# Optimization experiments

Hardware: AMD Instinct MI355X
Metric: run time of the kernel (lower is better)

Reference implementation:

```python
import jax, jax.numpy as jnp
import numpy as np

H, D, K = 8, 512, 64
EPS = 1e-12


def _l2norm(x):
    # F.normalize(p=2, dim=-1): x / max(||x||_2, eps)
    n = jnp.sqrt(jnp.sum(x * x, axis=-1, keepdims=True))
    return x / jnp.maximum(n, EPS)


def setup_inputs() -> dict:
    key = jax.random.key(0)
    ks = jax.random.split(key, 8)
    S, B = 1024, 16
    scale = 1.0 / np.sqrt(D)
    return {
        "query": jax.random.normal(ks[0], (S, B, D), dtype=jnp.float32),
        "key": jax.random.normal(ks[1], (S, B, D), dtype=jnp.float32),
        "value": jax.random.normal(ks[2], (S, B, D), dtype=jnp.float32),
        # stacked per-head projection weights, torch Linear convention [out,in]
        "WQ": jax.random.uniform(ks[3], (H, K, D), jnp.float32, -scale, scale),
        "WK": jax.random.uniform(ks[4], (H, K, D), jnp.float32, -scale, scale),
        "WV": jax.random.uniform(ks[5], (H, K, D), jnp.float32, -scale, scale),
        "Wout": jax.random.uniform(ks[6], (D, H * K), jnp.float32,
                                   -1.0 / np.sqrt(H * K), 1.0 / np.sqrt(H * K)),
    }


def reference(query, key, value, WQ, WK, WV, Wout):
    temp = K ** 0.5
    # project all heads at once: [S,B,D] x [H,K,D] -> [B,H,S,K]
    wq = _l2norm(jnp.einsum("sbd,hkd->bhsk", query, WQ))
    wk = _l2norm(jnp.einsum("sbd,hkd->bhsk", key, WK))
    wv = _l2norm(jnp.einsum("sbd,hkd->bhsk", value, WV))
    # cosine-similarity attention scores [B,H,Sq,Sk]
    scores = jnp.einsum("bhsk,bhtk->bhst", wq, wk) / temp
    aff = jax.nn.softmax(scores, axis=-1)
    out = jnp.einsum("bhst,bhtk->bhsk", aff, wv)  # [B,H,S,K]
    # concat heads -> [S,B,H*K] (matches torch per-head concat on last dim)
    Sq, B = query.shape[0], query.shape[1]
    concat = out.transpose(2, 0, 1, 3).reshape(Sq, B, H * K)
    return concat @ Wout.T  # [S,B,D]
```

## Files before the change

kernel.cpp:

```cpp
#include <hip/hip_runtime.h>
#include <cstdint>
#include <cstddef>

typedef unsigned int u32;
typedef unsigned short u16;
typedef __attribute__((ext_vector_type(8))) short short8;
typedef __attribute__((ext_vector_type(4))) float f32x4;

#define S_LEN 1024
#define BATCH 16
#define NHEAD 8
#define DMODEL 512
#define KHD 64
#define NROW (S_LEN * BATCH)

__device__ __forceinline__ u16 f2bf(float f) {
    u32 u = __float_as_uint(f);
    return (u16)((u + 0x7fffu + ((u >> 16) & 1u)) >> 16);
}

__device__ __forceinline__ void gl_lds16(const void* g, void* l) {
    __builtin_amdgcn_global_load_lds(
        (const __attribute__((address_space(1))) void*)(uintptr_t)g,
        (__attribute__((address_space(3))) void*)(uintptr_t)l, 16, 0, 0);
}

__global__ __launch_bounds__(256) void wcvt_kernel(
    const float* __restrict__ WQ, const float* __restrict__ WK,
    const float* __restrict__ WV, const float* __restrict__ Wo,
    u16* __restrict__ dst)
{
    const int m = blockIdx.y;
    const float* __restrict__ src = (m == 0) ? WQ : (m == 1) ? WK : (m == 2) ? WV : Wo;
    const int idx = (blockIdx.x * 256 + threadIdx.x) * 4;
    const float4 v = *(const float4*)(src + idx);
    u16 r[4];
    r[0] = f2bf(v.x); r[1] = f2bf(v.y); r[2] = f2bf(v.z); r[3] = f2bf(v.w);
    *(uint2*)(dst + (size_t)m * DMODEL * DMODEL + idx) = *(uint2*)r;
}

__global__ __launch_bounds__(512, 4) void proj_kernel(
    const float* __restrict__ q, const float* __restrict__ k,
    const float* __restrict__ v, const u16* __restrict__ Wb,
    u16* __restrict__ outN)
{
    __shared__ __align__(16) u16 Alds[2][128 * 64];
    __shared__ __align__(16) u16 Blds[2][128 * 64];

    const int tid  = threadIdx.x;
    const int wave = tid >> 6;
    const int lane = tid & 63;
    const int m16  = lane & 15;
    const int quad = lane >> 4;
    const int wm   = wave >> 1;
    const int wn   = wave & 1;

    const int bid  = blockIdx.x;
    const bool isM1 = bid < 1024;
    int z, bx, by, bb;
    if (isM1) { z = bid >> 9; by = (bid >> 7) & 3; bx = bid & 127; bb = 0; }
    else { const int r = bid - 1024; z = 2; bb = r >> 5; by = (r >> 3) & 3; bx = r & 7; }

    const int row0 = bx * 128;
    const int n0   = by * 128;
    const float* __restrict__ A32 = isM1 ? (z ? k : q) : (v + (size_t)bb * DMODEL);
    const size_t astr = isM1 ? (size_t)DMODEL : (size_t)BATCH * DMODEL;
    const u16* __restrict__ B = Wb + (size_t)z * DMODEL * DMODEL;

    f32x4 acc[2][4] = {};

    const int arow = wave * 16 + (lane >> 2);
    const int ac0  = lane & 3;
    const float* __restrict__ aPtr = A32 + (size_t)(row0 + arow) * astr;
    const int brow   = lane >> 3;
    const int bchunk = (lane & 7) ^ brow;

    float4 pA[4], pB[4];

#define LOADA(kt, rg)                                                           \
    {                                                                           \
        _Pragma("unroll")                                                       \
        for (int j = 0; j < 4; j++)                                             \
            rg[j] = *(const float4*)(aPtr + (kt) + (ac0 + 4 * j) * 4);          \
    }
#define WRITEA(rg, bufi)                                                        \
    {                                                                           \
        _Pragma("unroll")                                                       \
        for (int j = 0; j < 4; j++) {                                           \
            const int c = ac0 + 4 * j;                                          \
            u32 lo, hi;                                                         \
            asm("v_cvt_pk_bf16_f32 %0, %1, %2" : "=v"(lo) : "v"(rg[j].x), "v"(rg[j].y)); \
            asm("v_cvt_pk_bf16_f32 %0, %1, %2" : "=v"(hi) : "v"(rg[j].z), "v"(rg[j].w)); \
            uint2 pk; pk.x = lo; pk.y = hi;                                     \
            *(uint2*)&Alds[bufi][arow * 64 + (((c >> 1) ^ (arow & 7)) << 3) +   \
                                 ((c & 1) << 2)] = pk;                          \
        }                                                                       \
    }
#define STAGEB(kt, bufi)                                                        \
    {                                                                           \
        const u16* bp = B + (size_t)(n0 + wave * 16 + brow) * DMODEL + (kt) +   \
                        bchunk * 8;                                             \
        u16* lb = &Blds[bufi][(wave * 16) * 64];                                \
        gl_lds16(bp, lb);                                                       \
        gl_lds16(bp + (size_t)8 * DMODEL, lb + 8 * 64);                         \
    }

    auto compute = [&](int bufi) {
#pragma unroll
        for (int half = 0; half < 2; half++) {
            short8 af[2], bfr[4];
#pragma unroll
            for (int mt = 0; mt < 2; mt++)
                af[mt] = *(const short8*)&Alds[bufi][(wm * 32 + mt * 16 + m16) * 64 +
                                                     (((half << 2) + quad) ^ (m16 & 7)) * 8];
#pragma unroll
            for (int nt = 0; nt < 4; nt++)
                bfr[nt] = *(const short8*)&Blds[bufi][(wn * 64 + nt * 16 + m16) * 64 +
                                                      (((half << 2) + quad) ^ (m16 & 7)) * 8];
#pragma unroll
            for (int mt = 0; mt < 2; mt++)
#pragma unroll
                for (int nt = 0; nt < 4; nt++)
                    acc[mt][nt] = __builtin_amdgcn_mfma_f32_16x16x32_bf16(af[mt], bfr[nt], acc[mt][nt], 0, 0, 0);
        }
    };

    LOADA(0, pA)
    STAGEB(0, 0)
    LOADA(64, pB)
    STAGEB(64, 1)
    asm volatile("s_waitcnt vmcnt(6)" ::: "memory");
    __builtin_amdgcn_sched_barrier(0);
    WRITEA(pA, 0)
    asm volatile("s_waitcnt lgkmcnt(0)" ::: "memory");
    __builtin_amdgcn_s_barrier();
    __builtin_amdgcn_sched_barrier(0);

#pragma unroll
    for (int t = 0; t < 8; t++) {
        compute(t & 1);
        if (t < 6) {
            __builtin_amdgcn_s_barrier();
            __builtin_amdgcn_sched_barrier(0);
            if (t & 1) { LOADA((t + 2) * 64, pB) }
            else       { LOADA((t + 2) * 64, pA) }
            STAGEB((t + 2) * 64, t & 1);
        }
        if (t < 7) {
            if (t < 6) asm volatile("s_waitcnt vmcnt(6)" ::: "memory");
            else       asm volatile("s_waitcnt vmcnt(0)" ::: "memory");
            __builtin_amdgcn_sched_barrier(0);
            if ((t + 1) & 1) { WRITEA(pB, 1) }
            else             { WRITEA(pA, 0) }
            asm volatile("s_waitcnt lgkmcnt(0)" ::: "memory");
            __builtin_amdgcn_s_barrier();
            __builtin_amdgcn_sched_barrier(0);
        }
    }
#undef LOADA
#undef WRITEA
#undef STAGEB

    const int h = (n0 >> 6) + wn;
    u16* outZ = outN + (size_t)z * ((size_t)BATCH * NHEAD * S_LEN * KHD);
    if (isM1) {
#pragma unroll
        for (int mt = 0; mt < 2; mt++) {
#pragma unroll
            for (int r = 0; r < 4; r++) {
                float ss = 0.0f;
#pragma unroll
                for (int nt = 0; nt < 4; nt++) ss += acc[mt][nt][r] * acc[mt][nt][r];
                ss += __shfl_xor(ss, 1);
                ss += __shfl_xor(ss, 2);
                ss += __shfl_xor(ss, 4);
                ss += __shfl_xor(ss, 8);
                const float sc = 1.0f / fmaxf(sqrtf(ss), 1e-12f);
                const int i = row0 + wm * 32 + mt * 16 + quad * 4 + r;
                const int s = i >> 4, bq = i & 15;
                u16* op = outZ + (((size_t)bq * NHEAD + h) * S_LEN + s) * KHD;
#pragma unroll
                for (int nt = 0; nt < 4; nt++)
                    op[nt * 16 + m16] = f2bf(acc[mt][nt][r] * sc);
            }
        }
    } else {
#pragma unroll
        for (int mt = 0; mt < 2; mt++) {
            float scl[4];
#pragma unroll
            for (int r = 0; r < 4; r++) {
                float ss = 0.0f;
#pragma unroll
                for (int nt = 0; nt < 4; nt++) ss += acc[mt][nt][r] * acc[mt][nt][r];
                ss += __shfl_xor(ss, 1);
                ss += __shfl_xor(ss, 2);
                ss += __shfl_xor(ss, 4);
                ss += __shfl_xor(ss, 8);
                scl[r] = 1.0f / fmaxf(sqrtf(ss), 1e-12f);
            }
            const int sbase = row0 + wm * 32 + mt * 16 + quad * 4;
#pragma unroll
            for (int nt = 0; nt < 4; nt++) {
                const int vcol = nt * 16 + m16;
                uint2 pk;
                pk.x = (u32)f2bf(acc[mt][nt][0] * scl[0]) |
                       ((u32)f2bf(acc[mt][nt][1] * scl[1]) << 16);
                pk.y = (u32)f2bf(acc[mt][nt][2] * scl[2]) |
                       ((u32)f2bf(acc[mt][nt][3] * scl[3]) << 16);
                u16* dp = outZ + (((size_t)bb * NHEAD + h) * KHD + vcol) * S_LEN + sbase;
                *(uint2*)dp = pk;
            }
        }
    }
}

__global__ __launch_bounds__(512, 2) void gemm_out_kernel(
    const u16* __restrict__ Abf,
    const u16* __restrict__ Wb,
    float* __restrict__ outP)
{
    __shared__ __align__(16) u16 Alds[2][128 * 64];
    __shared__ __align__(16) u16 Blds[2][128 * 64];

    const int tid  = threadIdx.x;
    const int wave = tid >> 6;
    const int lane = tid & 63;
    const int m16  = lane & 15;
    const int quad = lane >> 4;
    const int wm   = wave >> 1;
    const int wn   = wave & 1;
    const int n0   = blockIdx.y * 128;
    const int row0 = blockIdx.x * 128;

    const int brow   = lane >> 3;
    const int bchunk = (lane & 7) ^ brow;

    f32x4 acc[2][4] = {};

    auto stage = [&](int kt, int b) {
        const int colc = kt + bchunk * 8;
        const int hh   = colc >> 6;
        const int kk   = colc & 63;
        u16* la = &Alds[b][(wave * 16) * 64];
#pragma unroll
        for (int j = 0; j < 2; j++) {
            const int i  = row0 + wave * 16 + j * 8 + brow;
            const int ss = i >> 4, bx = i & 15;
            gl_lds16(Abf + (((size_t)(bx * NHEAD + hh) * S_LEN + ss) * KHD + kk),
                     la + j * 8 * 64);
        }
        const u16* bp = Wb + (size_t)(n0 + wave * 16 + brow) * DMODEL + kt + bchunk * 8;
        u16* lb = &Blds[b][(wave * 16) * 64];
#pragma unroll
        for (int j = 0; j < 2; j++)
            gl_lds16(bp + (size_t)j * 8 * DMODEL, lb + j * 8 * 64);
    };
    auto compute = [&](int b) {
#pragma unroll
        for (int half = 0; half < 2; half++) {
            short8 af[2], bfr[4];
#pragma unroll
            for (int mt = 0; mt < 2; mt++)
                af[mt] = *(const short8*)&Alds[b][(wm * 32 + mt * 16 + m16) * 64 +
                                                  (((half << 2) + quad) ^ (m16 & 7)) * 8];
#pragma unroll
            for (int nt = 0; nt < 4; nt++)
                bfr[nt] = *(const short8*)&Blds[b][(wn * 64 + nt * 16 + m16) * 64 +
                                                   (((half << 2) + quad) ^ (m16 & 7)) * 8];
#pragma unroll
            for (int mt = 0; mt < 2; mt++)
#pragma unroll
                for (int nt = 0; nt < 4; nt++)
                    acc[mt][nt] = __builtin_amdgcn_mfma_f32_16x16x32_bf16(af[mt], bfr[nt], acc[mt][nt], 0, 0, 0);
        }
    };

    stage(0, 0);
    stage(64, 1);
    asm volatile("s_waitcnt vmcnt(4)" ::: "memory");
    __builtin_amdgcn_s_barrier();
    __builtin_amdgcn_sched_barrier(0);

#pragma unroll
    for (int t = 0; t < 8; t++) {
        compute(t & 1);
        if (t < 6) {
            __builtin_amdgcn_s_barrier();
            __builtin_amdgcn_sched_barrier(0);
            stage((t + 2) * 64, t & 1);
        }
        if (t < 7) {
            if (t < 6) asm volatile("s_waitcnt vmcnt(4)" ::: "memory");
            else       asm volatile("s_waitcnt vmcnt(0)" ::: "memory");
            __builtin_amdgcn_s_barrier();
            __builtin_amdgcn_sched_barrier(0);
        }
    }

#pragma unroll
    for (int mt = 0; mt < 2; mt++) {
#pragma unroll
        for (int r = 0; r < 4; r++) {
            const int i = row0 + wm * 32 + mt * 16 + quad * 4 + r;
            float* op = outP + (size_t)i * DMODEL + n0 + wn * 64;
#pragma unroll
            for (int nt = 0; nt < 4; nt++)
                op[nt * 16 + m16] = acc[mt][nt][r];
        }
    }
}

__global__ __launch_bounds__(256, 2) void attn_kernel(
    const u16* __restrict__ wq, const u16* __restrict__ wk, const u16* __restrict__ wvT,
    u16* __restrict__ Xout)
{
    __shared__ __align__(16) u16 Klds[2][64 * 64];
    __shared__ __align__(16) u16 Vlds[2][64 * 64];
    __shared__ __align__(16) u16 Plds[4][4][16 * 32];

    const int tid  = threadIdx.x;
    const int wave = tid >> 6;
    const int lane = tid & 63;
    const int m16  = lane & 15;
    const int quad = lane >> 4;
    const int bh   = blockIdx.x;
    const int qt   = blockIdx.y;

    const u16* Qb = wq  + (size_t)bh * S_LEN * KHD;
    const u16* Kb = wk  + (size_t)bh * S_LEN * KHD;
    const u16* Vb = wvT + (size_t)bh * KHD * S_LEN;

    const int qr0 = qt * 256 + wave * 64;
    short8 qf[4][2];
#pragma unroll
    for (int qb = 0; qb < 4; qb++) {
        qf[qb][0] = *(const short8*)(Qb + (size_t)(qr0 + qb * 16 + m16) * KHD + quad * 8);
        qf[qb][1] = *(const short8*)(Qb + (size_t)(qr0 + qb * 16 + m16) * KHD + 32 + quad * 8);
    }

    short8 ones;
#pragma unroll
    for (int j = 0; j < 8; j++) ones[j] = (short)0x3F80;

    f32x4 o[4][4] = {};
    f32x4 ls[4]   = {};
    const float C1 = 0.125f, C2 = 0.0078125f;

    const int srow   = lane >> 3;
    const int schunk = (lane & 7) ^ srow;
    const int r0     = wave * 8 + srow;
    const int pswz   = (m16 >> 1) & 3;

    gl_lds16(Kb + (size_t)r0 * KHD + schunk * 8,               &Klds[0][(wave * 8) * 64]);
    gl_lds16(Kb + (size_t)(r0 + 32) * KHD + schunk * 8,        &Klds[0][(wave * 8 + 32) * 64]);
    gl_lds16(Vb + (size_t)r0 * S_LEN + schunk * 8,             &Vlds[0][(wave * 8) * 64]);
    gl_lds16(Vb + (size_t)(r0 + 32) * S_LEN + schunk * 8,      &Vlds[0][(wave * 8 + 32) * 64]);
    __syncthreads();

    for (int it = 0; it < S_LEN / 64; it++) {
        const int cur = it & 1;

        if (it + 1 < S_LEN / 64) {
            const int nxt = cur ^ 1;
            const int kt0 = (it + 1) * 64;
            gl_lds16(Kb + (size_t)(kt0 + r0) * KHD + schunk * 8,        &Klds[nxt][(wave * 8) * 64]);
            gl_lds16(Kb + (size_t)(kt0 + r0 + 32) * KHD + schunk * 8,   &Klds[nxt][(wave * 8 + 32) * 64]);
            gl_lds16(Vb + (size_t)r0 * S_LEN + kt0 + schunk * 8,        &Vlds[nxt][(wave * 8) * 64]);
            gl_lds16(Vb + (size_t)(r0 + 32) * S_LEN + kt0 + schunk * 8, &Vlds[nxt][(wave * 8 + 32) * 64]);
        }

#pragma unroll
        for (int cc = 0; cc < 2; cc++) {
#pragma unroll
            for (int mm = 0; mm < 2; mm++) {
                const int mt = cc * 2 + mm;
                const short8 kf0 = *(const short8*)&Klds[cur][(mt * 16 + m16) * 64 + (quad ^ (m16 & 7)) * 8];
                const short8 kf1 = *(const short8*)&Klds[cur][(mt * 16 + m16) * 64 + ((4 + quad) ^ (m16 & 7)) * 8];
#pragma unroll
                for (int qb = 0; qb < 4; qb++) {
                    f32x4 s = {};
                    s = __builtin_amdgcn_mfma_f32_16x16x32_bf16(kf0, qf[qb][0], s, 0, 0, 0);
                    s = __builtin_amdgcn_mfma_f32_16x16x32_bf16(kf1, qf[qb][1], s, 0, 0, 0);
                    u32 up[4];
#pragma unroll
                    for (int r = 0; r < 4; r++) {
                        const float y = s[r];
                        const float p = fmaf(fmaf(C2, y, C1), y, 1.0f);
                        up[r] = __float_as_uint(p);
                    }
                    uint2 pk;
                    pk.x = __builtin_amdgcn_perm(up[1], up[0], 0x07060302u);
                    pk.y = __builtin_amdgcn_perm(up[3], up[2], 0x07060302u);
                    *(uint2*)((char*)&Plds[wave][qb][0] + m16 * 64 +
                              ((((mm << 1) + (quad >> 1)) ^ pswz) << 4) + ((quad & 1) << 3)) = pk;
                }
            }

            short8 vfr[4];
#pragma unroll
            for (int vt = 0; vt < 4; vt++)
                vfr[vt] = *(const short8*)&Vlds[cur][(vt * 16 + m16) * 64 +
                                                     (((cc << 2) + quad) ^ (m16 & 7)) * 8];
            __builtin_amdgcn_s_setprio(1);
#pragma unroll
            for (int qb = 0; qb < 4; qb++) {
                const short8 pb = *(const short8*)((const char*)&Plds[wave][qb][0] + m16 * 64 +
                                                   ((quad ^ pswz) << 4));
                ls[qb] = __builtin_amdgcn_mfma_f32_16x16x32_bf16(ones, pb, ls[qb], 0, 0, 0);
#pragma unroll
                for (int vt = 0; vt < 4; vt++)
                    o[qb][vt] = __builtin_amdgcn_mfma_f32_16x16x32_bf16(vfr[vt], pb, o[qb][vt], 0, 0, 0);
            }
            __builtin_amdgcn_s_setprio(0);
        }

        __syncthreads();
    }

    u16* outB = Xout + (size_t)bh * S_LEN * KHD;
#pragma unroll
    for (int qb = 0; qb < 4; qb++) {
        const float inv = 1.0f / ls[qb][0];
        const int qrow = qr0 + qb * 16 + m16;
        u16* cp = outB + (size_t)qrow * KHD;
#pragma unroll
        for (int vt = 0; vt < 4; vt++) {
            uint2 pk;
            pk.x = (u32)f2bf(o[qb][vt][0] * inv) | ((u32)f2bf(o[qb][vt][1] * inv) << 16);
            pk.y = (u32)f2bf(o[qb][vt][2] * inv) | ((u32)f2bf(o[qb][vt][3] * inv) << 16);
            *(uint2*)(cp + vt * 16 + quad * 4) = pk;
        }
    }
}

extern "C" void kernel_launch(void* const* d_in, const int* in_sizes, int n_in,
                              void* d_out, int out_size, void* d_ws, size_t ws_size,
                              hipStream_t stream) {
    const float* q    = (const float*)d_in[0];
    const float* k    = (const float*)d_in[1];
    const float* v    = (const float*)d_in[2];
    const float* WQ   = (const float*)d_in[3];
    const float* WK   = (const float*)d_in[4];
    const float* WV   = (const float*)d_in[5];
    const float* Wout = (const float*)d_in[6];
    float* out = (float*)d_out;

    const size_t per = (size_t)BATCH * NHEAD * S_LEN * KHD;
    u16* wsQKV = (u16*)d_ws;
    u16* wsW   = wsQKV + 3 * per;

    wcvt_kernel<<<dim3(256, 4), 256, 0, stream>>>(WQ, WK, WV, Wout, wsW);

    proj_kernel<<<dim3(1536), 512, 0, stream>>>(q, k, v, wsW, wsQKV);

    attn_kernel<<<dim3(BATCH * NHEAD, S_LEN / 256), 256, 0, stream>>>(
        wsQKV, wsQKV + per, wsQKV + 2 * per, wsQKV);

    gemm_out_kernel<<<dim3(NROW / 128, DMODEL / 128), 512, 0, stream>>>(
        wsQKV, wsW + (size_t)3 * DMODEL * DMODEL, out);
}
```

Before: 241.4 us.

## Fuse weight bf16 conversion into GEMM loaders and drop separate conversion kernel

```diff
diff --git a/kernel.cpp b/kernel.cpp
--- a/kernel.cpp
+++ b/kernel.cpp
@@ -25,23 +25,11 @@
         (__attribute__((address_space(3))) void*)(uintptr_t)l, 16, 0, 0);
 }
 
-__global__ __launch_bounds__(256) void wcvt_kernel(
-    const float* __restrict__ WQ, const float* __restrict__ WK,
-    const float* __restrict__ WV, const float* __restrict__ Wo,
-    u16* __restrict__ dst)
-{
-    const int m = blockIdx.y;
-    const float* __restrict__ src = (m == 0) ? WQ : (m == 1) ? WK : (m == 2) ? WV : Wo;
-    const int idx = (blockIdx.x * 256 + threadIdx.x) * 4;
-    const float4 v = *(const float4*)(src + idx);
-    u16 r[4];
-    r[0] = f2bf(v.x); r[1] = f2bf(v.y); r[2] = f2bf(v.z); r[3] = f2bf(v.w);
-    *(uint2*)(dst + (size_t)m * DMODEL * DMODEL + idx) = *(uint2*)r;
-}
-
 __global__ __launch_bounds__(512, 4) void proj_kernel(
     const float* __restrict__ q, const float* __restrict__ k,
-    const float* __restrict__ v, const u16* __restrict__ Wb,
+    const float* __restrict__ v,
+    const float* __restrict__ WQ, const float* __restrict__ WK,
+    const float* __restrict__ WV,
     u16* __restrict__ outN)
 {
     __shared__ __align__(16) u16 Alds[2][128 * 64];
@@ -65,50 +53,48 @@
     const int n0   = by * 128;
     const float* __restrict__ A32 = isM1 ? (z ? k : q) : (v + (size_t)bb * DMODEL);
     const size_t astr = isM1 ? (size_t)DMODEL : (size_t)BATCH * DMODEL;
-    const u16* __restrict__ B = Wb + (size_t)z * DMODEL * DMODEL;
+    const float* __restrict__ B32 = (z == 0) ? WQ : (z == 1) ? WK : WV;
 
     f32x4 acc[2][4] = {};
 
-    const int arow = wave * 16 + (lane >> 2);
-    const int ac0  = lane & 3;
-    const float* __restrict__ aPtr = A32 + (size_t)(row0 + arow) * astr;
-    const int brow   = lane >> 3;
-    const int bchunk = (lane & 7) ^ brow;
+    const int srow = wave * 16 + (lane >> 2);
+    const int sc0  = lane & 3;
+    const float* __restrict__ aPtr = A32 + (size_t)(row0 + srow) * astr;
+    const float* __restrict__ bPtr = B32 + (size_t)(n0 + srow) * DMODEL;
 
     float4 pA[4], pB[4];
+    float4 wA[4], wB[4];
 
 #define LOADA(kt, rg)                                                           \
     {                                                                           \
         _Pragma("unroll")                                                       \
         for (int j = 0; j < 4; j++)                                             \
-            rg[j] = *(const float4*)(aPtr + (kt) + (ac0 + 4 * j) * 4);          \
-    }
-#define WRITEA(rg, bufi)                                                        \
+            rg[j] = *(const float4*)(aPtr + (kt) + (sc0 + 4 * j) * 4);          \
+    }
+#define LOADB(kt, rg)                                                           \
+    {                                                                           \
+        _Pragma("unroll")                                                       \
+        for (int j = 0; j < 4; j++)                                             \
+            rg[j] = *(const float4*)(bPtr + (kt) + (sc0 + 4 * j) * 4);          \
+    }
+#define CVTWR(rg, lds, bufi)                                                    \
     {                                                                           \
         _Pragma("unroll")                                                       \
         for (int j = 0; j < 4; j++) {                                           \
-            const int c = ac0 + 4 * j;                                          \
+            const int c = sc0 + 4 * j;                                          \
             u32 lo, hi;                                                         \
             asm("v_cvt_pk_bf16_f32 %0, %1, %2" : "=v"(lo) : "v"(rg[j].x), "v"(rg[j].y)); \
             asm("v_cvt_pk_bf16_f32 %0, %1, %2" : "=v"(hi) : "v"(rg[j].z), "v"(rg[j].w)); \
             uint2 pk; pk.x = lo; pk.y = hi;                                     \
-            *(uint2*)&Alds[bufi][arow * 64 + (((c >> 1) ^ (arow & 7)) << 3) +   \
-                                 ((c & 1) << 2)] = pk;                          \
+            *(uint2*)&lds[bufi][srow * 64 + (((c >> 1) ^ (srow & 7)) << 3) +    \
+                               ((c & 1) << 2)] = pk;                            \
         }                                                                       \
     }
-#define STAGEB(kt, bufi)                                                        \
-    {                                                                           \
-        const u16* bp = B + (size_t)(n0 + wave * 16 + brow) * DMODEL + (kt) +   \
-                        bchunk * 8;                                             \
-        u16* lb = &Blds[bufi][(wave * 16) * 64];                                \
-        gl_lds16(bp, lb);                                                       \
-        gl_lds16(bp + (size_t)8 * DMODEL, lb + 8 * 64);                         \
-    }
 
     auto compute = [&](int bufi) {
+        short8 af[2], bfr[4];
 #pragma unroll
         for (int half = 0; half < 2; half++) {
-            short8 af[2], bfr[4];
 #pragma unroll
             for (int mt = 0; mt < 2; mt++)
                 af[mt] = *(const short8*)&Alds[bufi][(wm * 32 + mt * 16 + m16) * 64 +
@@ -117,21 +103,24 @@
             for (int nt = 0; nt < 4; nt++)
                 bfr[nt] = *(const short8*)&Blds[bufi][(wn * 64 + nt * 16 + m16) * 64 +
                                                       (((half << 2) + quad) ^ (m16 & 7)) * 8];
+            __builtin_amdgcn_s_setprio(1);
 #pragma unroll
             for (int mt = 0; mt < 2; mt++)
 #pragma unroll
                 for (int nt = 0; nt < 4; nt++)
                     acc[mt][nt] = __builtin_amdgcn_mfma_f32_16x16x32_bf16(af[mt], bfr[nt], acc[mt][nt], 0, 0, 0);
+            __builtin_amdgcn_s_setprio(0);
         }
     };
 
     LOADA(0, pA)
-    STAGEB(0, 0)
+    LOADB(0, wA)
     LOADA(64, pB)
-    STAGEB(64, 1)
-    asm volatile("s_waitcnt vmcnt(6)" ::: "memory");
+    LOADB(64, wB)
+    asm volatile("s_waitcnt vmcnt(8)" ::: "memory");
     __builtin_amdgcn_sched_barrier(0);
-    WRITEA(pA, 0)
+    CVTWR(pA, Alds, 0)
+    CVTWR(wA, Blds, 0)
     asm volatile("s_waitcnt lgkmcnt(0)" ::: "memory");
     __builtin_amdgcn_s_barrier();
     __builtin_amdgcn_sched_barrier(0);
@@ -142,24 +131,23 @@
         if (t < 6) {
             __builtin_amdgcn_s_barrier();
             __builtin_amdgcn_sched_barrier(0);
-            if (t & 1) { LOADA((t + 2) * 64, pB) }
-            else       { LOADA((t + 2) * 64, pA) }
-            STAGEB((t + 2) * 64, t & 1);
+            if (t & 1) { LOADA((t + 2) * 64, pB) LOADB((t + 2) * 64, wB) }
+            else       { LOADA((t + 2) * 64, pA) LOADB((t + 2) * 64, wA) }
         }
         if (t < 7) {
-            if (t < 6) asm volatile("s_waitcnt vmcnt(6)" ::: "memory");
+            if (t < 6) asm volatile("s_waitcnt vmcnt(8)" ::: "memory");
             else       asm volatile("s_waitcnt vmcnt(0)" ::: "memory");
             __builtin_amdgcn_sched_barrier(0);
-            if ((t + 1) & 1) { WRITEA(pB, 1) }
-            else             { WRITEA(pA, 0) }
+            if ((t + 1) & 1) { CVTWR(pB, Alds, 1) CVTWR(wB, Blds, 1) }
+            else             { CVTWR(pA, Alds, 0) CVTWR(wA, Blds, 0) }
             asm volatile("s_waitcnt lgkmcnt(0)" ::: "memory");
             __builtin_amdgcn_s_barrier();
             __builtin_amdgcn_sched_barrier(0);
         }
     }
 #undef LOADA
-#undef WRITEA
-#undef STAGEB
+#undef LOADB
+#undef CVTWR
 
     const int h = (n0 >> 6) + wn;
     u16* outZ = outN + (size_t)z * ((size_t)BATCH * NHEAD * S_LEN * KHD);
@@ -215,9 +203,9 @@
     }
 }
 
-__global__ __launch_bounds__(512, 2) void gemm_out_kernel(
+__global__ __launch_bounds__(512, 4) void gemm_out_kernel(
     const u16* __restrict__ Abf,
-    const u16* __restrict__ Wb,
+    const float* __restrict__ Wo32,
     float* __restrict__ outP)
 {
     __shared__ __align__(16) u16 Alds[2][128 * 64];
@@ -235,10 +223,14 @@
 
     const int brow   = lane >> 3;
     const int bchunk = (lane & 7) ^ brow;
+    const int srow = wave * 16 + (lane >> 2);
+    const int sc0  = lane & 3;
+    const float* __restrict__ bPtr = Wo32 + (size_t)(n0 + srow) * DMODEL;
 
     f32x4 acc[2][4] = {};
-
-    auto stage = [&](int kt, int b) {
+    float4 wA[4], wB[4];
+
+    auto stageA = [&](int kt, int b) {
         const int colc = kt + bchunk * 8;
         const int hh   = colc >> 6;
         const int kk   = colc & 63;
@@ -250,16 +242,30 @@
             gl_lds16(Abf + (((size_t)(bx * NHEAD + hh) * S_LEN + ss) * KHD + kk),
                      la + j * 8 * 64);
         }
-        const u16* bp = Wb + (size_t)(n0 + wave * 16 + brow) * DMODEL + kt + bchunk * 8;
-        u16* lb = &Blds[b][(wave * 16) * 64];
-#pragma unroll
-        for (int j = 0; j < 2; j++)
-            gl_lds16(bp + (size_t)j * 8 * DMODEL, lb + j * 8 * 64);
     };
+#define LOADB(kt, rg)                                                           \
+    {                                                                           \
+        _Pragma("unroll")                                                       \
+        for (int j = 0; j < 4; j++)                                             \
+            rg[j] = *(const float4*)(bPtr + (kt) + (sc0 + 4 * j) * 4);          \
+    }
+#define CVTWRB(rg, bufi)                                                        \
+    {                                                                           \
+        _Pragma("unroll")                                                       \
+        for (int j = 0; j < 4; j++) {                                           \
+            const int c = sc0 + 4 * j;                                          \
+            u32 lo, hi;                                                         \
+            asm("v_cvt_pk_bf16_f32 %0, %1, %2" : "=v"(lo) : "v"(rg[j].x), "v"(rg[j].y)); \
+            asm("v_cvt_pk_bf16_f32 %0, %1, %2" : "=v"(hi) : "v"(rg[j].z), "v"(rg[j].w)); \
+            uint2 pk; pk.x = lo; pk.y = hi;                                     \
+            *(uint2*)&Blds[bufi][srow * 64 + (((c >> 1) ^ (srow & 7)) << 3) +   \
+                                 ((c & 1) << 2)] = pk;                          \
+        }                                                                       \
+    }
     auto compute = [&](int b) {
+        short8 af[2], bfr[4];
 #pragma unroll
         for (int half = 0; half < 2; half++) {
-            short8 af[2], bfr[4];
 #pragma unroll
             for (int mt = 0; mt < 2; mt++)
                 af[mt] = *(const short8*)&Alds[b][(wm * 32 + mt * 16 + m16) * 64 +
@@ -268,17 +274,24 @@
             for (int nt = 0; nt < 4; nt++)
                 bfr[nt] = *(const short8*)&Blds[b][(wn * 64 + nt * 16 + m16) * 64 +
                                                    (((half << 2) + quad) ^ (m16 & 7)) * 8];
+            __builtin_amdgcn_s_setprio(1);
 #pragma unroll
             for (int mt = 0; mt < 2; mt++)
 #pragma unroll
                 for (int nt = 0; nt < 4; nt++)
                     acc[mt][nt] = __builtin_amdgcn_mfma_f32_16x16x32_bf16(af[mt], bfr[nt], acc[mt][nt], 0, 0, 0);
+            __builtin_amdgcn_s_setprio(0);
         }
     };
 
-    stage(0, 0);
-    stage(64, 1);
-    asm volatile("s_waitcnt vmcnt(4)" ::: "memory");
+    stageA(0, 0);
+    LOADB(0, wA)
+    stageA(64, 1);
+    LOADB(64, wB)
+    asm volatile("s_waitcnt vmcnt(6)" ::: "memory");
+    __builtin_amdgcn_sched_barrier(0);
+    CVTWRB(wA, 0)
+    asm volatile("s_waitcnt lgkmcnt(0)" ::: "memory");
     __builtin_amdgcn_s_barrier();
     __builtin_amdgcn_sched_barrier(0);
 
@@ -288,15 +301,23 @@
         if (t < 6) {
             __builtin_amdgcn_s_barrier();
             __builtin_amdgcn_sched_barrier(0);
-            stage((t + 2) * 64, t & 1);
+            stageA((t + 2) * 64, t & 1);
+            if (t & 1) { LOADB((t + 2) * 64, wB) }
+            else       { LOADB((t + 2) * 64, wA) }
         }
         if (t < 7) {
-            if (t < 6) asm volatile("s_waitcnt vmcnt(4)" ::: "memory");
+            if (t < 6) asm volatile("s_waitcnt vmcnt(6)" ::: "memory");
             else       asm volatile("s_waitcnt vmcnt(0)" ::: "memory");
+            __builtin_amdgcn_sched_barrier(0);
+            if ((t + 1) & 1) { CVTWRB(wB, 1) }
+            else             { CVTWRB(wA, 0) }
+            asm volatile("s_waitcnt lgkmcnt(0)" ::: "memory");
             __builtin_amdgcn_s_barrier();
             __builtin_amdgcn_sched_barrier(0);
         }
     }
+#undef LOADB
+#undef CVTWRB
 
 #pragma unroll
     for (int mt = 0; mt < 2; mt++) {
@@ -448,15 +469,12 @@
 
     const size_t per = (size_t)BATCH * NHEAD * S_LEN * KHD;
     u16* wsQKV = (u16*)d_ws;
-    u16* wsW   = wsQKV + 3 * per;
-
-    wcvt_kernel<<<dim3(256, 4), 256, 0, stream>>>(WQ, WK, WV, Wout, wsW);
-
-    proj_kernel<<<dim3(1536), 512, 0, stream>>>(q, k, v, wsW, wsQKV);
+
+    proj_kernel<<<dim3(1536), 512, 0, stream>>>(q, k, v, WQ, WK, WV, wsQKV);
 
     attn_kernel<<<dim3(BATCH * NHEAD, S_LEN / 256), 256, 0, stream>>>(
         wsQKV, wsQKV + per, wsQKV + 2 * per, wsQKV);
 
     gemm_out_kernel<<<dim3(NROW / 128, DMODEL / 128), 512, 0, stream>>>(
-        wsQKV, wsW + (size_t)3 * DMODEL * DMODEL, out);
-}
+        wsQKV, Wout, out);
+}
```

Result: slower. 246.5 us (+2.1%).
